# Kernel optimization log

Measured on AMD Instinct MI355X. Metric: run time of the kernel, lower is better.

Reference implementation:

```python
import jax, jax.numpy as jnp
import numpy as np

B, N, KNB, F, H = 1, 50000, 16, 128, 128
BN_EPS = 1e-3  # keras BatchNormalization default epsilon
ALPHA = 0.3    # keras LeakyReLU default negative slope


def setup_inputs() -> dict:
    key = jax.random.key(0)
    ks = jax.random.split(key, 14)
    s_in = 1.0 / np.sqrt(F)
    s_cat = 1.0 / np.sqrt(F + H)
    return {
        'embeddings': jax.random.normal(ks[0], (B, N, F), jnp.float32),
        'weights': jnp.zeros((1, 1), jnp.float32),  # unused in call_att
        'neighbor_set': jax.random.randint(ks[1], (B, N, KNB), 0, N),
        'Wq': jax.random.normal(ks[2], (F, H), jnp.float32) * s_in,
        'bq': jnp.zeros((H,), jnp.float32),
        'Wk': jax.random.normal(ks[3], (F, H), jnp.float32) * s_in,
        'bk': jnp.zeros((H,), jnp.float32),
        'Wv': jax.random.normal(ks[4], (F, H), jnp.float32) * s_in,
        'bv': jnp.zeros((H,), jnp.float32),
        'W1': jax.random.normal(ks[5], (F + H, H), jnp.float32) * s_cat,
        'b1': jnp.zeros((H,), jnp.float32),
        'gamma': 1.0 + 0.1 * jax.random.normal(ks[6], (H,), jnp.float32),
        'beta': 0.1 * jax.random.normal(ks[7], (H,), jnp.float32),
        'mov_mean': 0.1 * jax.random.normal(ks[8], (H,), jnp.float32),
        'mov_var': 1.0 + 0.1 * jax.random.uniform(ks[9], (H,), jnp.float32),
    }


def reference(embeddings, weights, neighbor_set, Wq, bq, Wk, bk, Wv, bv,
              W1, b1, gamma, beta, mov_mean, mov_var):
    lrelu = lambda x: jax.nn.leaky_relu(x, ALPHA)
    # batched gather: nb[b, n, k] = embeddings[b, neighbor_set[b, n, k]]  -> [B,N,K,F]
    nb = jax.vmap(lambda e, idx: e[idx])(embeddings, neighbor_set)
    q = lrelu(embeddings @ Wq + bq)      # [B,N,H]
    k = lrelu(nb @ Wk + bk)              # [B,N,K,H]
    v = lrelu(nb @ Wv + bv)              # [B,N,K,H]
    # Q is tiled across the K neighbor rows in the original; every attention row
    # is identical, so mean-pool over rows == single-query attention. Same math.
    scores = jnp.einsum('bnh,bnkh->bnk', q, k)          # dot-product, no scale
    attn = jax.nn.softmax(scores, axis=-1)
    pooled = jnp.einsum('bnk,bnkh->bnh', attn, v)       # [B,N,H]
    h = lrelu(jnp.concatenate([embeddings, pooled], axis=-1) @ W1 + b1)
    h = h / (jnp.linalg.norm(h, axis=2, keepdims=True) + 1e-6)
    # BatchNormalization (inference form, axis=-1)
    return gamma * (h - mov_mean) * jax.lax.rsqrt(mov_var + BN_EPS) + beta
```

## Files before the change

kernel.cpp:

```cpp
#include <hip/hip_runtime.h>
#include <hip/hip_bf16.h>

#define N_NODES 50000
#define KNB 16
#define FDIM 128
#define HDIM 128
#define ALPHA 0.3f
#define BN_EPS 1e-3f

typedef __bf16 v8bf __attribute__((ext_vector_type(8)));
typedef float v4f __attribute__((ext_vector_type(4)));
typedef unsigned short ushort_t;

__device__ __forceinline__ float blo(unsigned int u) {
    union { float f; unsigned int i; } x; x.i = u << 16; return x.f;
}
__device__ __forceinline__ float bhi(unsigned int u) {
    union { float f; unsigned int i; } x; x.i = u & 0xffff0000u; return x.f;
}

__device__ __forceinline__ unsigned short f2bf(float f) {
    union { float f; unsigned int u; } x;
    x.f = f;
    unsigned int r = x.u + 0x7fffu + ((x.u >> 16) & 1u);
    return (unsigned short)(r >> 16);
}

__device__ __forceinline__ unsigned int pk2(float a, float b) {
    __hip_bfloat162 h = __float22bfloat162_rn(make_float2(a, b));
    union { __hip_bfloat162 h; unsigned int u; } r; r.h = h; return r.u;
}

__device__ __forceinline__ float lrelu(float x) { return x > 0.f ? x : ALPHA * x; }

__device__ __forceinline__ v8bf load8f(const float* p) {
    float4 A = ((const float4*)p)[0];
    float4 B = ((const float4*)p)[1];
    union { v8bf v; unsigned int u[4]; } r;
    r.u[0] = pk2(A.x, A.y); r.u[1] = pk2(A.z, A.w);
    r.u[2] = pk2(B.x, B.y); r.u[3] = pk2(B.z, B.w);
    return r.v;
}

__global__ __launch_bounds__(256) void prep_kernel(
    const float* __restrict__ Wq, const float* __restrict__ Wk,
    const float* __restrict__ Wv, const float* __restrict__ W1,
    ushort_t* __restrict__ WT)
{
    const int idx = blockIdx.x * 256 + threadIdx.x;
    if (idx < 16384) {
        int k = idx >> 7, n = idx & 127;
        WT[n * 128 + k] = f2bf(Wq[idx]);
    } else if (idx < 32768) {
        int i = idx - 16384; int k = i >> 7, n = i & 127;
        WT[16384 + n * 128 + k] = f2bf(Wk[i]);
    } else if (idx < 49152) {
        int i = idx - 32768; int k = i >> 7, n = i & 127;
        WT[32768 + n * 128 + k] = f2bf(Wv[i]);
    } else if (idx < 81920) {
        int i = idx - 49152; int k = i >> 7, n = i & 127;
        WT[49152 + n * 256 + k] = f2bf(W1[i]);
    }
}

__global__ __launch_bounds__(256) void qkv_kernel(
    const float* __restrict__ E, const ushort_t* __restrict__ WT,
    const float* __restrict__ bq, const float* __restrict__ bk,
    const float* __restrict__ bv,
    float* __restrict__ Qo, ushort_t* __restrict__ KV)
{
    __shared__ ushort_t sW[128 * 136];

    const int tid  = threadIdx.x;
    const int wave = tid >> 6;
    const int lane = tid & 63;
    const int quad = lane >> 4;
    const int j    = lane & 15;
    const int row0 = blockIdx.x * 128 + wave * 32;

    const int ar0 = min(row0 + j,      N_NODES - 1);
    const int ar1 = min(row0 + 16 + j, N_NODES - 1);

    v8bf a0f[4], a1f[4];
#pragma unroll
    for (int ks = 0; ks < 4; ++ks) {
        const int k0 = ks * 32 + quad * 8;
        a0f[ks] = load8f(E + (size_t)ar0 * FDIM + k0);
        a1f[ks] = load8f(E + (size_t)ar1 * FDIM + k0);
    }

    const float* biases[3] = {bq, bk, bv};

    for (int w = 0; w < 3; ++w) {
        const ushort_t* Wsrc = WT + w * 16384;
        for (int i = tid; i < 2048; i += 256) {
            int n = i >> 4, kc = i & 15;
            *(uint4*)(&sW[n * 136 + kc * 8]) = *(const uint4*)(Wsrc + n * 128 + kc * 8);
        }
        __syncthreads();

        v4f acc[2][8];
#pragma unroll
        for (int rb = 0; rb < 2; ++rb)
#pragma unroll
            for (int c = 0; c < 8; ++c) acc[rb][c] = (v4f){0.f, 0.f, 0.f, 0.f};

#pragma unroll
        for (int ks = 0; ks < 4; ++ks) {
            const int k0 = ks * 32 + quad * 8;
            v8bf b[8];
#pragma unroll
            for (int c = 0; c < 8; ++c)
                b[c] = *(const v8bf*)(&sW[(c * 16 + j) * 136 + k0]);
#pragma unroll
            for (int c = 0; c < 8; ++c) {
                acc[0][c] = __builtin_amdgcn_mfma_f32_16x16x32_bf16(a0f[ks], b[c], acc[0][c], 0, 0, 0);
                acc[1][c] = __builtin_amdgcn_mfma_f32_16x16x32_bf16(a1f[ks], b[c], acc[1][c], 0, 0, 0);
            }
        }

        const float* bias = biases[w];
#pragma unroll
        for (int c = 0; c < 8; ++c) {
            const int col = c * 16 + j;
            const float bv_ = bias[col];
#pragma unroll
            for (int rb = 0; rb < 2; ++rb) {
#pragma unroll
                for (int i = 0; i < 4; ++i) {
                    const int r = row0 + rb * 16 + quad * 4 + i;
                    if (r < N_NODES) {
                        const float x = lrelu(acc[rb][c][i] + bv_);
                        if (w == 0)      Qo[(size_t)r * HDIM + col] = x;
                        else if (w == 1) KV[(size_t)r * 256 + col] = f2bf(x);
                        else             KV[(size_t)r * 256 + 128 + col] = f2bf(x);
                    }
                }
            }
        }
        __syncthreads();
    }
}

__global__ __launch_bounds__(256) void attn_kernel(
    float* __restrict__ QP, const ushort_t* __restrict__ KV,
    const int* __restrict__ nbr)
{
    __shared__ float sE[4 * 16];

    const int tid  = threadIdx.x;
    const int wave = tid >> 6;
    const int lane = tid & 63;
    const int node = __builtin_amdgcn_readfirstlane(blockIdx.x * 4 + wave);

    const int t = lane >> 2;
    const int s = lane & 3;

    const int* nb = nbr + node * KNB;
    int idt = nb[t];
    idt = ((unsigned)idt < (unsigned)N_NODES) ? idt : 0;

    const uint4* kbase = (const uint4*)(KV + (size_t)idt * 256 + s * 32);
    uint4 kk[4];
#pragma unroll
    for (int i = 0; i < 4; ++i) kk[i] = kbase[i];

    const float4* qbase = (const float4*)(QP + (size_t)node * HDIM + s * 32);
    float4 qv[8];
#pragma unroll
    for (int i = 0; i < 8; ++i) qv[i] = qbase[i];

    float p = 0.f;
#pragma unroll
    for (int i = 0; i < 4; ++i) {
        const float4 qa = qv[2 * i], qb = qv[2 * i + 1];
        p += qa.x * blo(kk[i].x) + qa.y * bhi(kk[i].x)
           + qa.z * blo(kk[i].y) + qa.w * bhi(kk[i].y)
           + qb.x * blo(kk[i].z) + qb.y * bhi(kk[i].z)
           + qb.z * blo(kk[i].w) + qb.w * bhi(kk[i].w);
    }
    p += __shfl_xor(p, 1, 64);
    p += __shfl_xor(p, 2, 64);

    float m = p;
    m = fmaxf(m, __shfl_xor(m, 4, 64));
    m = fmaxf(m, __shfl_xor(m, 8, 64));
    m = fmaxf(m, __shfl_xor(m, 16, 64));
    m = fmaxf(m, __shfl_xor(m, 32, 64));

    const float e = __expf(p - m);
    if (s == 0) sE[wave * 16 + t] = e;
    __syncthreads();

    float ear[16];
#pragma unroll
    for (int i = 0; i < 4; ++i)
        ((float4*)ear)[i] = ((const float4*)(sE + wave * 16))[i];
    float sum = 0.f;
#pragma unroll
    for (int tt = 0; tt < KNB; ++tt) sum += ear[tt];
    const float inv = 1.f / sum;

    float p0 = 0.f, p1 = 0.f;
#pragma unroll
    for (int tt = 0; tt < KNB; ++tt) {
        int id = nb[tt];
        id = ((unsigned)id < (unsigned)N_NODES) ? id : 0;
        const unsigned int vp = *(const unsigned int*)(KV + (size_t)id * 256 + 128 + 2 * lane);
        p0 += ear[tt] * blo(vp);
        p1 += ear[tt] * bhi(vp);
    }
    ((float2*)(QP + (size_t)node * HDIM))[lane] = make_float2(p0 * inv, p1 * inv);
}

__global__ __launch_bounds__(256) void out_kernel(
    const float* __restrict__ E, const ushort_t* __restrict__ W1T,
    const float* __restrict__ b1,
    const float* __restrict__ gamma, const float* __restrict__ beta,
    const float* __restrict__ mmean, const float* __restrict__ mvar,
    float* __restrict__ OutP)
{
    __shared__ ushort_t sW[128 * 136];

    const int tid  = threadIdx.x;
    const int wave = tid >> 6;
    const int lane = tid & 63;
    const int quad = lane >> 4;
    const int j    = lane & 15;
    const int row0 = blockIdx.x * 128 + wave * 32;

    const int ar0 = min(row0 + j,      N_NODES - 1);
    const int ar1 = min(row0 + 16 + j, N_NODES - 1);

    v4f acc[2][8];
#pragma unroll
    for (int rb = 0; rb < 2; ++rb)
#pragma unroll
        for (int c = 0; c < 8; ++c) acc[rb][c] = (v4f){0.f, 0.f, 0.f, 0.f};

    for (int half = 0; half < 2; ++half) {
        for (int i = tid; i < 2048; i += 256) {
            int n = i >> 4, kc = i & 15;
            *(uint4*)(&sW[n * 136 + kc * 8]) =
                *(const uint4*)(W1T + n * 256 + half * 128 + kc * 8);
        }
        __syncthreads();

        const float* Abase = (half == 0) ? E : (const float*)OutP;
#pragma unroll
        for (int ks = 0; ks < 4; ++ks) {
            const int k0 = ks * 32 + quad * 8;
            v8bf a0 = load8f(Abase + (size_t)ar0 * 128 + k0);
            v8bf a1 = load8f(Abase + (size_t)ar1 * 128 + k0);
            v8bf b[8];
#pragma unroll
            for (int c = 0; c < 8; ++c)
                b[c] = *(const v8bf*)(&sW[(c * 16 + j) * 136 + k0]);
#pragma unroll
            for (int c = 0; c < 8; ++c) {
                acc[0][c] = __builtin_amdgcn_mfma_f32_16x16x32_bf16(a0, b[c], acc[0][c], 0, 0, 0);
                acc[1][c] = __builtin_amdgcn_mfma_f32_16x16x32_bf16(a1, b[c], acc[1][c], 0, 0, 0);
            }
        }
        __syncthreads();
    }

    float scale_[8], shift_[8], bias_[8];
#pragma unroll
    for (int c = 0; c < 8; ++c) {
        const int col = c * 16 + j;
        const float sc = gamma[col] * rsqrtf(mvar[col] + BN_EPS);
        scale_[c] = sc;
        shift_[c] = beta[col] - mmean[col] * sc;
        bias_[c]  = b1[col];
    }

#pragma unroll
    for (int rb = 0; rb < 2; ++rb)
#pragma unroll
        for (int c = 0; c < 8; ++c)
#pragma unroll
            for (int i = 0; i < 4; ++i)
                acc[rb][c][i] = lrelu(acc[rb][c][i] + bias_[c]);

#pragma unroll
    for (int rb = 0; rb < 2; ++rb) {
#pragma unroll
        for (int i = 0; i < 4; ++i) {
            float ss = 0.f;
#pragma unroll
            for (int c = 0; c < 8; ++c) ss += acc[rb][c][i] * acc[rb][c][i];
            ss += __shfl_xor(ss, 1, 64);
            ss += __shfl_xor(ss, 2, 64);
            ss += __shfl_xor(ss, 4, 64);
            ss += __shfl_xor(ss, 8, 64);
            const float invn = 1.f / (sqrtf(ss) + 1e-6f);
            const int r = row0 + rb * 16 + quad * 4 + i;
            if (r < N_NODES) {
#pragma unroll
                for (int c = 0; c < 8; ++c) {
                    OutP[(size_t)r * HDIM + c * 16 + j] =
                        acc[rb][c][i] * invn * scale_[c] + shift_[c];
                }
            }
        }
    }
}

extern "C" void kernel_launch(void* const* d_in, const int* in_sizes, int n_in,
                              void* d_out, int out_size, void* d_ws, size_t ws_size,
                              hipStream_t stream)
{
    const float* E     = (const float*)d_in[0];
    const int*   nbr   = (const int*)d_in[2];
    const float* Wq    = (const float*)d_in[3];
    const float* bq    = (const float*)d_in[4];
    const float* Wk    = (const float*)d_in[5];
    const float* bk    = (const float*)d_in[6];
    const float* Wv    = (const float*)d_in[7];
    const float* bv    = (const float*)d_in[8];
    const float* W1    = (const float*)d_in[9];
    const float* b1    = (const float*)d_in[10];
    const float* gam   = (const float*)d_in[11];
    const float* bet   = (const float*)d_in[12];
    const float* mmean = (const float*)d_in[13];
    const float* mvar  = (const float*)d_in[14];

    ushort_t* KV = (ushort_t*)d_ws;
    ushort_t* WT = KV + (size_t)N_NODES * 256;
    float* QP = (float*)d_out;

    const int gridA = (N_NODES + 127) / 128;
    prep_kernel<<<320, 256, 0, stream>>>(Wq, Wk, Wv, W1, WT);
    qkv_kernel<<<gridA, 256, 0, stream>>>(E, WT, bq, bk, bv, QP, KV);
    attn_kernel<<<N_NODES / 4, 256, 0, stream>>>(QP, KV, nbr);
    out_kernel<<<gridA, 256, 0, stream>>>(E, WT + 49152, b1, gam, bet, mmean, mvar, QP);
}
```

Before: 229.9 us.

## Halve GEMM row tiles and replace LDS softmax exchange with wave shuffles

The qkv and out GEMM kernels now give each wave 16 rows instead of 32, so each block covers 64 rows. That doubles the grid to about 782 blocks, which fills the CUs better and lowers per-thread accumulator registers, at the cost of loading the weight tile into LDS twice as often in total. The attention kernel drops its shared-memory exchange and __syncthreads for softmax weights and uses cross-lane shuffles for the sum and the per-neighbor weights. It also issues all 16 V-row gathers at the top so they overlap with the score computation, which costs extra registers.

```diff
diff --git a/kernel.cpp b/kernel.cpp
--- a/kernel.cpp
+++ b/kernel.cpp
@@ -76,18 +76,14 @@
     const int lane = tid & 63;
     const int quad = lane >> 4;
     const int j    = lane & 15;
-    const int row0 = blockIdx.x * 128 + wave * 32;
-
-    const int ar0 = min(row0 + j,      N_NODES - 1);
-    const int ar1 = min(row0 + 16 + j, N_NODES - 1);
-
-    v8bf a0f[4], a1f[4];
-#pragma unroll
-    for (int ks = 0; ks < 4; ++ks) {
-        const int k0 = ks * 32 + quad * 8;
-        a0f[ks] = load8f(E + (size_t)ar0 * FDIM + k0);
-        a1f[ks] = load8f(E + (size_t)ar1 * FDIM + k0);
-    }
+    const int row0 = blockIdx.x * 64 + wave * 16;
+
+    const int ar = min(row0 + j, N_NODES - 1);
+
+    v8bf af[4];
+#pragma unroll
+    for (int ks = 0; ks < 4; ++ks)
+        af[ks] = load8f(E + (size_t)ar * FDIM + ks * 32 + quad * 8);
 
     const float* biases[3] = {bq, bk, bv};
 
@@ -99,11 +95,9 @@
         }
         __syncthreads();
 
-        v4f acc[2][8];
-#pragma unroll
-        for (int rb = 0; rb < 2; ++rb)
-#pragma unroll
-            for (int c = 0; c < 8; ++c) acc[rb][c] = (v4f){0.f, 0.f, 0.f, 0.f};
+        v4f acc[8];
+#pragma unroll
+        for (int c = 0; c < 8; ++c) acc[c] = (v4f){0.f, 0.f, 0.f, 0.f};
 
 #pragma unroll
         for (int ks = 0; ks < 4; ++ks) {
@@ -113,10 +107,8 @@
             for (int c = 0; c < 8; ++c)
                 b[c] = *(const v8bf*)(&sW[(c * 16 + j) * 136 + k0]);
 #pragma unroll
-            for (int c = 0; c < 8; ++c) {
-                acc[0][c] = __builtin_amdgcn_mfma_f32_16x16x32_bf16(a0f[ks], b[c], acc[0][c], 0, 0, 0);
-                acc[1][c] = __builtin_amdgcn_mfma_f32_16x16x32_bf16(a1f[ks], b[c], acc[1][c], 0, 0, 0);
-            }
+            for (int c = 0; c < 8; ++c)
+                acc[c] = __builtin_amdgcn_mfma_f32_16x16x32_bf16(af[ks], b[c], acc[c], 0, 0, 0);
         }
 
         const float* bias = biases[w];
@@ -125,16 +117,13 @@
             const int col = c * 16 + j;
             const float bv_ = bias[col];
 #pragma unroll
-            for (int rb = 0; rb < 2; ++rb) {
-#pragma unroll
-                for (int i = 0; i < 4; ++i) {
-                    const int r = row0 + rb * 16 + quad * 4 + i;
-                    if (r < N_NODES) {
-                        const float x = lrelu(acc[rb][c][i] + bv_);
-                        if (w == 0)      Qo[(size_t)r * HDIM + col] = x;
-                        else if (w == 1) KV[(size_t)r * 256 + col] = f2bf(x);
-                        else             KV[(size_t)r * 256 + 128 + col] = f2bf(x);
-                    }
+            for (int i = 0; i < 4; ++i) {
+                const int r = row0 + quad * 4 + i;
+                if (r < N_NODES) {
+                    const float x = lrelu(acc[c][i] + bv_);
+                    if (w == 0)      Qo[(size_t)r * HDIM + col] = x;
+                    else if (w == 1) KV[(size_t)r * 256 + col] = f2bf(x);
+                    else             KV[(size_t)r * 256 + 128 + col] = f2bf(x);
                 }
             }
         }
@@ -146,8 +135,6 @@
     float* __restrict__ QP, const ushort_t* __restrict__ KV,
     const int* __restrict__ nbr)
 {
-    __shared__ float sE[4 * 16];
-
     const int tid  = threadIdx.x;
     const int wave = tid >> 6;
     const int lane = tid & 63;
@@ -157,9 +144,17 @@
     const int s = lane & 3;
 
     const int* nb = nbr + node * KNB;
+
+    unsigned int vvals[KNB];
+#pragma unroll
+    for (int tt = 0; tt < KNB; ++tt) {
+        int id = nb[tt];
+        id = ((unsigned)id < (unsigned)N_NODES) ? id : 0;
+        vvals[tt] = *(const unsigned int*)(KV + (size_t)id * 256 + 128 + 2 * lane);
+    }
+
     int idt = nb[t];
     idt = ((unsigned)idt < (unsigned)N_NODES) ? idt : 0;
-
     const uint4* kbase = (const uint4*)(KV + (size_t)idt * 256 + s * 32);
     uint4 kk[4];
 #pragma unroll
@@ -189,26 +184,20 @@
     m = fmaxf(m, __shfl_xor(m, 32, 64));
 
     const float e = __expf(p - m);
-    if (s == 0) sE[wave * 16 + t] = e;
-    __syncthreads();
-
-    float ear[16];
-#pragma unroll
-    for (int i = 0; i < 4; ++i)
-        ((float4*)ear)[i] = ((const float4*)(sE + wave * 16))[i];
-    float sum = 0.f;
-#pragma unroll
-    for (int tt = 0; tt < KNB; ++tt) sum += ear[tt];
+
+    float sum = e;
+    sum += __shfl_xor(sum, 4, 64);
+    sum += __shfl_xor(sum, 8, 64);
+    sum += __shfl_xor(sum, 16, 64);
+    sum += __shfl_xor(sum, 32, 64);
     const float inv = 1.f / sum;
 
     float p0 = 0.f, p1 = 0.f;
 #pragma unroll
     for (int tt = 0; tt < KNB; ++tt) {
-        int id = nb[tt];
-        id = ((unsigned)id < (unsigned)N_NODES) ? id : 0;
-        const unsigned int vp = *(const unsigned int*)(KV + (size_t)id * 256 + 128 + 2 * lane);
-        p0 += ear[tt] * blo(vp);
-        p1 += ear[tt] * bhi(vp);
+        const float a = __shfl(e, 4 * tt, 64);
+        p0 += a * blo(vvals[tt]);
+        p1 += a * bhi(vvals[tt]);
     }
     ((float2*)(QP + (size_t)node * HDIM))[lane] = make_float2(p0 * inv, p1 * inv);
 }
@@ -227,16 +216,13 @@
     const int lane = tid & 63;
     const int quad = lane >> 4;
     const int j    = lane & 15;
-    const int row0 = blockIdx.x * 128 + wave * 32;
-
-    const int ar0 = min(row0 + j,      N_NODES - 1);
-    const int ar1 = min(row0 + 16 + j, N_NODES - 1);
-
-    v4f acc[2][8];
-#pragma unroll
-    for (int rb = 0; rb < 2; ++rb)
-#pragma unroll
-        for (int c = 0; c < 8; ++c) acc[rb][c] = (v4f){0.f, 0.f, 0.f, 0.f};
+    const int row0 = blockIdx.x * 64 + wave * 16;
+
+    const int ar = min(row0 + j, N_NODES - 1);
+
+    v4f acc[8];
+#pragma unroll
+    for (int c = 0; c < 8; ++c) acc[c] = (v4f){0.f, 0.f, 0.f, 0.f};
 
     for (int half = 0; half < 2; ++half) {
         for (int i = tid; i < 2048; i += 256) {
@@ -250,17 +236,14 @@
 #pragma unroll
         for (int ks = 0; ks < 4; ++ks) {
             const int k0 = ks * 32 + quad * 8;
-            v8bf a0 = load8f(Abase + (size_t)ar0 * 128 + k0);
-            v8bf a1 = load8f(Abase + (size_t)ar1 * 128 + k0);
+            v8bf a = load8f(Abase + (size_t)ar * 128 + k0);
             v8bf b[8];
 #pragma unroll
             for (int c = 0; c < 8; ++c)
                 b[c] = *(const v8bf*)(&sW[(c * 16 + j) * 136 + k0]);
 #pragma unroll
-            for (int c = 0; c < 8; ++c) {
-                acc[0][c] = __builtin_amdgcn_mfma_f32_16x16x32_bf16(a0, b[c], acc[0][c], 0, 0, 0);
-                acc[1][c] = __builtin_amdgcn_mfma_f32_16x16x32_bf16(a1, b[c], acc[1][c], 0, 0, 0);
-            }
+            for (int c = 0; c < 8; ++c)
+                acc[c] = __builtin_amdgcn_mfma_f32_16x16x32_bf16(a, b[c], acc[c], 0, 0, 0);
         }
         __syncthreads();
     }
@@ -276,33 +259,27 @@
     }
 
 #pragma unroll
-    for (int rb = 0; rb < 2; ++rb)
-#pragma unroll
-        for (int c = 0; c < 8; ++c)
-#pragma unroll
-            for (int i = 0; i < 4; ++i)
-                acc[rb][c][i] = lrelu(acc[rb][c][i] + bias_[c]);
-
-#pragma unroll
-    for (int rb = 0; rb < 2; ++rb) {
-#pragma unroll
-        for (int i = 0; i < 4; ++i) {
-            float ss = 0.f;
-#pragma unroll
-            for (int c = 0; c < 8; ++c) ss += acc[rb][c][i] * acc[rb][c][i];
-            ss += __shfl_xor(ss, 1, 64);
-            ss += __shfl_xor(ss, 2, 64);
-            ss += __shfl_xor(ss, 4, 64);
-            ss += __shfl_xor(ss, 8, 64);
-            const float invn = 1.f / (sqrtf(ss) + 1e-6f);
-            const int r = row0 + rb * 16 + quad * 4 + i;
-            if (r < N_NODES) {
-#pragma unroll
-                for (int c = 0; c < 8; ++c) {
-                    OutP[(size_t)r * HDIM + c * 16 + j] =
-                        acc[rb][c][i] * invn * scale_[c] + shift_[c];
-                }
-            }
+    for (int c = 0; c < 8; ++c)
+#pragma unroll
+        for (int i = 0; i < 4; ++i)
+            acc[c][i] = lrelu(acc[c][i] + bias_[c]);
+
+#pragma unroll
+    for (int i = 0; i < 4; ++i) {
+        float ss = 0.f;
+#pragma unroll
+        for (int c = 0; c < 8; ++c) ss += acc[c][i] * acc[c][i];
+        ss += __shfl_xor(ss, 1, 64);
+        ss += __shfl_xor(ss, 2, 64);
+        ss += __shfl_xor(ss, 4, 64);
+        ss += __shfl_xor(ss, 8, 64);
+        const float invn = 1.f / (sqrtf(ss) + 1e-6f);
+        const int r = row0 + quad * 4 + i;
+        if (r < N_NODES) {
+#pragma unroll
+            for (int c = 0; c < 8; ++c)
+                OutP[(size_t)r * HDIM + c * 16 + j] =
+                    acc[c][i] * invn * scale_[c] + shift_[c];
         }
     }
 }
@@ -330,7 +307,7 @@
     ushort_t* WT = KV + (size_t)N_NODES * 256;
     float* QP = (float*)d_out;
 
-    const int gridA = (N_NODES + 127) / 128;
+    const int gridA = (N_NODES + 63) / 64;
     prep_kernel<<<320, 256, 0, stream>>>(Wq, Wk, Wv, W1, WT);
     qkv_kernel<<<gridA, 256, 0, stream>>>(E, WT, bq, bk, bv, QP, KV);
     attn_kernel<<<N_NODES / 4, 256, 0, stream>>>(QP, KV, nbr);
```

Result: slower. 236.2 us (+2.7%).
